# Kernel optimization log

Measured on AMD Instinct MI355X. Metric: run time of the kernel, lower is better.

Reference implementation:

```python
import jax, jax.numpy as jnp
import numpy as np

B, N, DIN, DOUT = 8, 2048, 512, 512
EDGE_P = 0.01  # edge probability for the random binary adjacency


def setup_inputs() -> dict:
    key = jax.random.key(0)
    k1, k2, k3, k4 = jax.random.split(key, 4)
    inputs = jax.random.normal(k1, (B, N, DIN), dtype=jnp.float32)
    # binary dense adjacency (dense_to_sparse discards weights -> edges are adj != 0)
    adj = (jax.random.uniform(k2, (B, N, N)) < EDGE_P).astype(jnp.float32)
    W = jax.random.normal(k3, (DIN, DOUT), dtype=jnp.float32) / np.sqrt(DIN)
    b = jax.random.normal(k4, (DOUT,), dtype=jnp.float32) * 0.01
    return {"inputs": inputs, "adj": adj, "W": W, "b": b}


def _gcn_norm(adj):
    # binary edge mask (edge weights from dense_to_sparse are discarded)
    A = (adj != 0).astype(adj.dtype)
    # add remaining self-loops: force diagonal to 1
    eye = jnp.eye(A.shape[-1], dtype=A.dtype)
    A = jnp.maximum(A, eye)
    deg = A.sum(axis=-1)                       # [B, N]
    dinv = jnp.where(deg > 0, jax.lax.rsqrt(deg), 0.0)
    # D^-1/2 (A + I) D^-1/2
    return dinv[..., :, None] * A * dinv[..., None, :]


def reference(inputs, adj, W, b):
    norm = _gcn_norm(adj)                      # [B, N, N]
    h = jnp.einsum('bnf,fo->bno', inputs, W)   # linear (no internal bias)
    agg = jnp.einsum('bnm,bmo->bno', norm, h)  # degree-normalized aggregation
    return jnp.tanh(agg + b)
```

## Files before the change

kernel.cpp:

```cpp
#include <hip/hip_runtime.h>
#include <hip/hip_bf16.h>
#include <math.h>


#define NROWS 16384
#define NCOLS 2048
#define DF    512
#define CAP   64

typedef __attribute__((ext_vector_type(8))) short bf16x8;
typedef __attribute__((ext_vector_type(4))) float f32x4;
typedef const void __attribute__((address_space(1))) gvoid_t;
typedef void __attribute__((address_space(3))) svoid_t;

__global__ __launch_bounds__(256) void scan_wt_cvt(
    const float* __restrict__ W, __hip_bfloat16* __restrict__ WT,
    const float* __restrict__ adj, int* __restrict__ cnt,
    int* __restrict__ edges, float* __restrict__ dinv,
    const float* __restrict__ X, __hip_bfloat16* __restrict__ Xb) {
  __shared__ float t[64][65];
  const int blk = blockIdx.x;
  const int tid = threadIdx.x;
  if (blk < 64) {
    const int bx = blk & 7, by = blk >> 3;
    const int tx = tid & 63, ty = tid >> 6;
    #pragma unroll
    for (int i = 0; i < 16; ++i)
      t[ty + i * 4][tx] = W[(size_t)(by * 64 + ty + i * 4) * DF + bx * 64 + tx];
    __syncthreads();
    #pragma unroll
    for (int i = 0; i < 16; ++i)
      WT[(size_t)(bx * 64 + ty + i * 4) * DF + by * 64 + tx] =
          __float2bfloat16(t[tx][ty + i * 4]);
    return;
  }
  if (blk >= 1088) {
    const int b = blk - 1088;
    const float4* X4 = (const float4*)X;
    ushort4* O4 = (ushort4*)Xb;
    #pragma unroll
    for (int i = 0; i < 4; ++i) {
      const int idx = b * 1024 + i * 256 + tid;
      const float4 v = X4[idx];
      union { ushort4 u; __hip_bfloat16 h[4]; } p;
      p.h[0] = __float2bfloat16(v.x);
      p.h[1] = __float2bfloat16(v.y);
      p.h[2] = __float2bfloat16(v.z);
      p.h[3] = __float2bfloat16(v.w);
      O4[idx] = p.u;
    }
    return;
  }
  const int lane = tid & 63;
  const int wv = tid >> 6;
  const int rbase = (blk - 64) * 16 + wv * 4;
  float4 cur[8], nxt[8];
  {
    const float4* r4 = (const float4*)(adj + (size_t)rbase * NCOLS);
    #pragma unroll
    for (int k = 0; k < 8; ++k) cur[k] = r4[k * 64 + lane];
  }
  #pragma unroll
  for (int g = 0; g < 4; ++g) {
    const int r = rbase + g;
    if (g < 3) {
      const float4* rn = (const float4*)(adj + (size_t)(r + 1) * NCOLS);
      #pragma unroll
      for (int k = 0; k < 8; ++k) nxt[k] = rn[k * 64 + lane];
    }
    const int n = r & (NCOLS - 1);
    unsigned m = 0;
    #pragma unroll
    for (int k = 0; k < 8; ++k) {
      m |= (cur[k].x != 0.0f ? 1u : 0u) << (4 * k);
      m |= (cur[k].y != 0.0f ? 1u : 0u) << (4 * k + 1);
      m |= (cur[k].z != 0.0f ? 1u : 0u) << (4 * k + 2);
      m |= (cur[k].w != 0.0f ? 1u : 0u) << (4 * k + 3);
    }
    if (lane == ((n >> 2) & 63))
      m |= 1u << (((n >> 8) << 2) | (n & 3));
    const int c_ = __popc(m);
    int inc = c_;
    #pragma unroll
    for (int off = 1; off < 64; off <<= 1) {
      const int tv = __shfl_up(inc, off);
      if (lane >= off) inc += tv;
    }
    const int tot = __shfl(inc, 63);
    int p = inc - c_;
    unsigned mm = m;
    const size_t eb = (size_t)r * CAP;
    while (mm) {
      const int bpos = __ffs(mm) - 1;
      mm &= mm - 1;
      if (p < CAP)
        edges[eb + p] = ((bpos >> 2) << 8) + (lane << 2) + (bpos & 3);
      ++p;
    }
    if (lane == 63) {
      cnt[r] = tot < CAP ? tot : CAP;
      dinv[r] = rsqrtf((float)tot);
    }
    #pragma unroll
    for (int k = 0; k < 8; ++k) cur[k] = nxt[k];
  }
}

__global__ __launch_bounds__(256) void gemm_k(
    const __hip_bfloat16* __restrict__ A, const __hip_bfloat16* __restrict__ BT,
    __hip_bfloat16* __restrict__ H) {
  __shared__ __hip_bfloat16 As[2][128 * 32];
  __shared__ __hip_bfloat16 Bs[2][128 * 32];
  const int tid = threadIdx.x;
  const int lane = tid & 63;
  const int w = tid >> 6;
  const int id = blockIdx.x;
  const int xcd = id & 7;
  const int jj = id >> 3;
  const int bm = (xcd * 16 + (jj >> 2)) * 128;
  const int bn = (jj & 3) * 128;

  const int wm = (w >> 1) * 64;
  const int wn = (w & 1) * 64;
  const int srow = tid >> 2;
  const int scol = (tid & 3) * 8;
  const int kl = (lane >> 4) * 8;
  const int rl = lane & 15;

  f32x4 acc[4][4] = {};

  #define STAGE(k0, buf)  do {                                          \
    _Pragma("unroll")                                                   \
    for (int i = 0; i < 2; ++i) {                                       \
      const __hip_bfloat16* ga = A  + (size_t)(bm + i * 64 + srow) * DF + (k0) + scol; \
      const __hip_bfloat16* gb = BT + (size_t)(bn + i * 64 + srow) * DF + (k0) + scol; \
      char* la = (char*)&As[buf][0] + i * 4096 + w * 1024;              \
      char* lb = (char*)&Bs[buf][0] + i * 4096 + w * 1024;              \
      __builtin_amdgcn_global_load_lds((gvoid_t*)ga, (svoid_t*)la, 16, 0, 0); \
      __builtin_amdgcn_global_load_lds((gvoid_t*)gb, (svoid_t*)lb, 16, 0, 0); \
    } } while (0)

  STAGE(0, 0);
  __syncthreads();

  for (int tIt = 0; tIt < 16; ++tIt) {
    const int c_ = tIt & 1, nx = c_ ^ 1;
    if (tIt < 15) STAGE((tIt + 1) * 32, nx);
    bf16x8 af[4], bf[4];
    #pragma unroll
    for (int mi = 0; mi < 4; ++mi)
      af[mi] = *(const bf16x8*)&As[c_][(wm + mi * 16 + rl) * 32 + kl];
    #pragma unroll
    for (int ni = 0; ni < 4; ++ni)
      bf[ni] = *(const bf16x8*)&Bs[c_][(wn + ni * 16 + rl) * 32 + kl];
    #pragma unroll
    for (int mi = 0; mi < 4; ++mi)
      #pragma unroll
      for (int ni = 0; ni < 4; ++ni)
        acc[mi][ni] = __builtin_amdgcn_mfma_f32_16x16x32_bf16(af[mi], bf[ni], acc[mi][ni], 0, 0, 0);
    __syncthreads();
  }

  const int rq = (lane >> 4) * 4;
  #pragma unroll
  for (int mi = 0; mi < 4; ++mi)
    #pragma unroll
    for (int ni = 0; ni < 4; ++ni) {
      const int col = bn + wn + ni * 16 + rl;
      #pragma unroll
      for (int j = 0; j < 4; ++j) {
        const int row = bm + wm + mi * 16 + rq + j;
        H[(size_t)row * DF + col] = __float2bfloat16(acc[mi][ni][j]);
      }
    }
  #undef STAGE
}

__global__ __launch_bounds__(256) void aggregate(
    const __hip_bfloat16* __restrict__ h, const int* __restrict__ cnt,
    const int* __restrict__ edges, const float* __restrict__ dinv,
    const float* __restrict__ bias, float* __restrict__ out) {
  const int lane = threadIdx.x & 63;
  const int wv = threadIdx.x >> 6;
  const int batch = blockIdx.x & 7;
  const int qb = blockIdx.x >> 3;
  const int r0n = qb * 8 + wv * 2;
  const int r0 = (batch << 11) + r0n;
  const int r1 = r0 + 1;
  const float* dv = dinv + (batch << 11);
  const uint4* hbase = (const uint4*)(h + (size_t)(batch << 11) * DF);

  const int c0 = cnt[r0], c1 = cnt[r1];
  int   ml0 = 0, ml1 = 0;
  float wl0 = 0.0f, wl1 = 0.0f;
  if (lane < c0) { ml0 = edges[(size_t)r0 * CAP + lane]; wl0 = dv[ml0]; }
  if (lane < c1) { ml1 = edges[(size_t)r1 * CAP + lane]; wl1 = dv[ml1]; }

  float a0[8] = {0.f,0.f,0.f,0.f,0.f,0.f,0.f,0.f};
  float a1[8] = {0.f,0.f,0.f,0.f,0.f,0.f,0.f,0.f};
  const int cmax = c0 > c1 ? c0 : c1;
  for (int e = 0; e < cmax; e += 4) {
    uint4 v0[4], v1[4];
    #pragma unroll
    for (int j = 0; j < 4; ++j) {
      if (e + j < c0) v0[j] = hbase[(size_t)__shfl(ml0, e + j) * 64 + lane];
      if (e + j < c1) v1[j] = hbase[(size_t)__shfl(ml1, e + j) * 64 + lane];
    }
    #pragma unroll
    for (int j = 0; j < 4; ++j) {
      if (e + j < c0) {
        const float wt = __shfl(wl0, e + j);
        a0[0] += wt * __uint_as_float(v0[j].x << 16);
        a0[1] += wt * __uint_as_float(v0[j].x & 0xffff0000u);
        a0[2] += wt * __uint_as_float(v0[j].y << 16);
        a0[3] += wt * __uint_as_float(v0[j].y & 0xffff0000u);
        a0[4] += wt * __uint_as_float(v0[j].z << 16);
        a0[5] += wt * __uint_as_float(v0[j].z & 0xffff0000u);
        a0[6] += wt * __uint_as_float(v0[j].w << 16);
        a0[7] += wt * __uint_as_float(v0[j].w & 0xffff0000u);
      }
      if (e + j < c1) {
        const float wt = __shfl(wl1, e + j);
        a1[0] += wt * __uint_as_float(v1[j].x << 16);
        a1[1] += wt * __uint_as_float(v1[j].x & 0xffff0000u);
        a1[2] += wt * __uint_as_float(v1[j].y << 16);
        a1[3] += wt * __uint_as_float(v1[j].y & 0xffff0000u);
        a1[4] += wt * __uint_as_float(v1[j].z << 16);
        a1[5] += wt * __uint_as_float(v1[j].z & 0xffff0000u);
        a1[6] += wt * __uint_as_float(v1[j].w << 16);
        a1[7] += wt * __uint_as_float(v1[j].w & 0xffff0000u);
      }
    }
  }
  const float4* b4 = (const float4*)bias;
  const float4 bb0 = b4[lane * 2];
  const float4 bb1 = b4[lane * 2 + 1];
  const float dn0 = dv[r0n], dn1 = dv[r0n + 1];
  float4 o;
  float* op0 = out + (size_t)r0 * DF + lane * 8;
  o.x = tanhf(a0[0] * dn0 + bb0.x); o.y = tanhf(a0[1] * dn0 + bb0.y);
  o.z = tanhf(a0[2] * dn0 + bb0.z); o.w = tanhf(a0[3] * dn0 + bb0.w);
  *(float4*)op0 = o;
  o.x = tanhf(a0[4] * dn0 + bb1.x); o.y = tanhf(a0[5] * dn0 + bb1.y);
  o.z = tanhf(a0[6] * dn0 + bb1.z); o.w = tanhf(a0[7] * dn0 + bb1.w);
  *(float4*)(op0 + 4) = o;
  float* op1 = out + (size_t)r1 * DF + lane * 8;
  o.x = tanhf(a1[0] * dn1 + bb0.x); o.y = tanhf(a1[1] * dn1 + bb0.y);
  o.z = tanhf(a1[2] * dn1 + bb0.z); o.w = tanhf(a1[3] * dn1 + bb0.w);
  *(float4*)op1 = o;
  o.x = tanhf(a1[4] * dn1 + bb1.x); o.y = tanhf(a1[5] * dn1 + bb1.y);
  o.z = tanhf(a1[6] * dn1 + bb1.z); o.w = tanhf(a1[7] * dn1 + bb1.w);
  *(float4*)(op1 + 4) = o;
}

extern "C" void kernel_launch(void* const* d_in, const int* in_sizes, int n_in,
                              void* d_out, int out_size, void* d_ws, size_t ws_size,
                              hipStream_t stream) {
  const float* X    = (const float*)d_in[0];
  const float* adj  = (const float*)d_in[1];
  const float* W    = (const float*)d_in[2];
  const float* bias = (const float*)d_in[3];
  float* out = (float*)d_out;

  char* ws = (char*)d_ws;
  __hip_bfloat16* h    = (__hip_bfloat16*)(ws);
  __hip_bfloat16* WT   = (__hip_bfloat16*)(ws + 16777216);
  float*          dinv = (float*)(ws + 17301504);
  int*            cnt  = (int*)  (ws + 17367040);
  int*            edges= (int*)  (ws + 17432576);
  __hip_bfloat16* Xb   = (__hip_bfloat16*)(ws + 21626880);

  scan_wt_cvt<<<3136, 256, 0, stream>>>(W, WT, adj, cnt, edges, dinv, X, Xb);
  gemm_k<<<512, 256, 0, stream>>>(Xb, WT, h);
  aggregate<<<2048, 256, 0, stream>>>(h, cnt, edges, dinv, bias, out);
}
```

Baseline: 82.22 us.

## Assign one row per wave in aggregate, unroll gathers by 8, use fast tanh

The aggregation kernel now gives each wavefront a single output row instead of two, which doubles the grid and removes the divergence from handling two rows with different edge counts. Edge indices and degree weights are read directly with scalar-uniform loads rather than loaded per lane and broadcast through shuffles. The gather loop is unrolled by 8 to keep more loads in flight. tanhf is replaced by an exp/fast-divide formula, which is less accurate and may overflow to a wrong edge value for very large inputs.

```diff
diff --git a/kernel.cpp b/kernel.cpp
--- a/kernel.cpp
+++ b/kernel.cpp
@@ -176,6 +176,11 @@
   #undef STAGE
 }
 
+__device__ __forceinline__ float fast_tanh(float x) {
+  const float t = __expf(2.0f * x);
+  return 1.0f - __fdividef(2.0f, t + 1.0f);
+}
+
 __global__ __launch_bounds__(256) void aggregate(
     const __hip_bfloat16* __restrict__ h, const int* __restrict__ cnt,
     const int* __restrict__ edges, const float* __restrict__ dinv,
@@ -184,73 +189,57 @@
   const int wv = threadIdx.x >> 6;
   const int batch = blockIdx.x & 7;
   const int qb = blockIdx.x >> 3;
-  const int r0n = qb * 8 + wv * 2;
-  const int r0 = (batch << 11) + r0n;
-  const int r1 = r0 + 1;
+  const int rn = qb * 4 + wv;
+  const int r = (batch << 11) + rn;
+  const int c = cnt[r];
   const float* dv = dinv + (batch << 11);
   const uint4* hbase = (const uint4*)(h + (size_t)(batch << 11) * DF);
-
-  const int c0 = cnt[r0], c1 = cnt[r1];
-  int   ml0 = 0, ml1 = 0;
-  float wl0 = 0.0f, wl1 = 0.0f;
-  if (lane < c0) { ml0 = edges[(size_t)r0 * CAP + lane]; wl0 = dv[ml0]; }
-  if (lane < c1) { ml1 = edges[(size_t)r1 * CAP + lane]; wl1 = dv[ml1]; }
-
-  float a0[8] = {0.f,0.f,0.f,0.f,0.f,0.f,0.f,0.f};
-  float a1[8] = {0.f,0.f,0.f,0.f,0.f,0.f,0.f,0.f};
-  const int cmax = c0 > c1 ? c0 : c1;
-  for (int e = 0; e < cmax; e += 4) {
-    uint4 v0[4], v1[4];
-    #pragma unroll
-    for (int j = 0; j < 4; ++j) {
-      if (e + j < c0) v0[j] = hbase[(size_t)__shfl(ml0, e + j) * 64 + lane];
-      if (e + j < c1) v1[j] = hbase[(size_t)__shfl(ml1, e + j) * 64 + lane];
-    }
-    #pragma unroll
-    for (int j = 0; j < 4; ++j) {
-      if (e + j < c0) {
-        const float wt = __shfl(wl0, e + j);
-        a0[0] += wt * __uint_as_float(v0[j].x << 16);
-        a0[1] += wt * __uint_as_float(v0[j].x & 0xffff0000u);
-        a0[2] += wt * __uint_as_float(v0[j].y << 16);
-        a0[3] += wt * __uint_as_float(v0[j].y & 0xffff0000u);
-        a0[4] += wt * __uint_as_float(v0[j].z << 16);
-        a0[5] += wt * __uint_as_float(v0[j].z & 0xffff0000u);
-        a0[6] += wt * __uint_as_float(v0[j].w << 16);
-        a0[7] += wt * __uint_as_float(v0[j].w & 0xffff0000u);
+  const int* eb = edges + (size_t)r * CAP;
+
+  float acc[8] = {0.f,0.f,0.f,0.f,0.f,0.f,0.f,0.f};
+  for (int e = 0; e < c; e += 8) {
+    int   mj[8];
+    float wj[8];
+    uint4 vj[8];
+    #pragma unroll
+    for (int j = 0; j < 8; ++j)
+      if (e + j < c) mj[j] = eb[e + j];
+    #pragma unroll
+    for (int j = 0; j < 8; ++j)
+      if (e + j < c) {
+        wj[j] = dv[mj[j]];
+        vj[j] = hbase[(size_t)mj[j] * 64 + lane];
       }
-      if (e + j < c1) {
-        const float wt = __shfl(wl1, e + j);
-        a1[0] += wt * __uint_as_float(v1[j].x << 16);
-        a1[1] += wt * __uint_as_float(v1[j].x & 0xffff0000u);
-        a1[2] += wt * __uint_as_float(v1[j].y << 16);
-        a1[3] += wt * __uint_as_float(v1[j].y & 0xffff0000u);
-        a1[4] += wt * __uint_as_float(v1[j].z << 16);
-        a1[5] += wt * __uint_as_float(v1[j].z & 0xffff0000u);
-        a1[6] += wt * __uint_as_float(v1[j].w << 16);
-        a1[7] += wt * __uint_as_float(v1[j].w & 0xffff0000u);
+    #pragma unroll
+    for (int j = 0; j < 8; ++j)
+      if (e + j < c) {
+        const float wt = wj[j];
+        acc[0] += wt * __uint_as_float(vj[j].x << 16);
+        acc[1] += wt * __uint_as_float(vj[j].x & 0xffff0000u);
+        acc[2] += wt * __uint_as_float(vj[j].y << 16);
+        acc[3] += wt * __uint_as_float(vj[j].y & 0xffff0000u);
+        acc[4] += wt * __uint_as_float(vj[j].z << 16);
+        acc[5] += wt * __uint_as_float(vj[j].z & 0xffff0000u);
+        acc[6] += wt * __uint_as_float(vj[j].w << 16);
+        acc[7] += wt * __uint_as_float(vj[j].w & 0xffff0000u);
       }
-    }
   }
   const float4* b4 = (const float4*)bias;
   const float4 bb0 = b4[lane * 2];
   const float4 bb1 = b4[lane * 2 + 1];
-  const float dn0 = dv[r0n], dn1 = dv[r0n + 1];
+  const float dn = dv[rn];
   float4 o;
-  float* op0 = out + (size_t)r0 * DF + lane * 8;
-  o.x = tanhf(a0[0] * dn0 + bb0.x); o.y = tanhf(a0[1] * dn0 + bb0.y);
-  o.z = tanhf(a0[2] * dn0 + bb0.z); o.w = tanhf(a0[3] * dn0 + bb0.w);
-  *(float4*)op0 = o;
-  o.x = tanhf(a0[4] * dn0 + bb1.x); o.y = tanhf(a0[5] * dn0 + bb1.y);
-  o.z = tanhf(a0[6] * dn0 + bb1.z); o.w = tanhf(a0[7] * dn0 + bb1.w);
-  *(float4*)(op0 + 4) = o;
-  float* op1 = out + (size_t)r1 * DF + lane * 8;
-  o.x = tanhf(a1[0] * dn1 + bb0.x); o.y = tanhf(a1[1] * dn1 + bb0.y);
-  o.z = tanhf(a1[2] * dn1 + bb0.z); o.w = tanhf(a1[3] * dn1 + bb0.w);
-  *(float4*)op1 = o;
-  o.x = tanhf(a1[4] * dn1 + bb1.x); o.y = tanhf(a1[5] * dn1 + bb1.y);
-  o.z = tanhf(a1[6] * dn1 + bb1.z); o.w = tanhf(a1[7] * dn1 + bb1.w);
-  *(float4*)(op1 + 4) = o;
+  float* op = out + (size_t)r * DF + lane * 8;
+  o.x = fast_tanh(acc[0] * dn + bb0.x);
+  o.y = fast_tanh(acc[1] * dn + bb0.y);
+  o.z = fast_tanh(acc[2] * dn + bb0.z);
+  o.w = fast_tanh(acc[3] * dn + bb0.w);
+  *(float4*)op = o;
+  o.x = fast_tanh(acc[4] * dn + bb1.x);
+  o.y = fast_tanh(acc[5] * dn + bb1.y);
+  o.z = fast_tanh(acc[6] * dn + bb1.z);
+  o.w = fast_tanh(acc[7] * dn + bb1.w);
+  *(float4*)(op + 4) = o;
 }
 
 extern "C" void kernel_launch(void* const* d_in, const int* in_sizes, int n_in,
@@ -272,5 +261,5 @@
 
   scan_wt_cvt<<<3136, 256, 0, stream>>>(W, WT, adj, cnt, edges, dinv, X, Xb);
   gemm_k<<<512, 256, 0, stream>>>(Xb, WT, h);
-  aggregate<<<2048, 256, 0, stream>>>(h, cnt, edges, dinv, bias, out);
-}
+  aggregate<<<4096, 256, 0, stream>>>(h, cnt, edges, dinv, bias, out);
+}
```

Result: faster. 72.55 us (-11.8%).
